# Kernel optimization log

Measured on AMD Instinct MI355X. Metric: run time of the kernel, lower is better.

The kernel has to match this reference:

```python
import math
import jax, jax.numpy as jnp
import numpy as np

NUM_HEADS = 16
ROTARY_BASE = 10000.0
FMIN = -3.4028234663852886e+38  # torch uses -FLT_MAX as the blocked logit value


def setup_inputs() -> dict:
    key = jax.random.key(0)
    ks = jax.random.split(key, 4)
    B, S, D = 2, 2048, 2048
    x = jax.random.normal(ks[0], (B, S, D), dtype=jnp.float32)
    mask = jnp.ones((B, S), dtype=bool)
    # Linear params stored as [in, out] (transpose of torch's [out, in])
    w_in = jax.random.normal(ks[1], (D, 3 * D), dtype=jnp.float32) * 0.02
    b_in = jnp.zeros((3 * D,), dtype=jnp.float32)
    w_out = jax.random.normal(ks[2], (D, D), dtype=jnp.float32) * 0.02
    b_out = jnp.zeros((D,), dtype=jnp.float32)
    return {"x": x, "mask": mask, "w_in": w_in, "b_in": b_in,
            "w_out": w_out, "b_out": b_out}


def _rotate_half(t):
    # curated-transformers RotaryEmbeddings._rotate: [-x2, x1]
    h = t.shape[-1] // 2
    return jnp.concatenate([-t[..., h:], t[..., :h]], axis=-1)


def _rope_cos_sin(seq_len, width):
    # theta_i = base^(-2i/d); m_theta duplicated (rotate-half / NeoX layout)
    theta = ROTARY_BASE ** (-jnp.arange(0, width, 2, dtype=jnp.float32) / width)
    m_theta = jnp.arange(seq_len, dtype=jnp.float32)[:, None] * theta[None, :]
    m_theta = jnp.concatenate([m_theta, m_theta], axis=-1)  # [S, width]
    return jnp.cos(m_theta), jnp.sin(m_theta)


def reference(x, mask, w_in, b_in, w_out, b_out):
    B, S, D = x.shape
    H = NUM_HEADS
    Dh = D // H

    proj = x @ w_in + b_in                       # [B, S, 3D]
    q, k, v = jnp.split(proj, 3, axis=-1)
    split = lambda t: t.reshape(B, S, H, Dh).transpose(0, 2, 1, 3)  # [B,H,S,Dh]
    q, k, v = split(q), split(k), split(v)

    # rotary_fraction == 1.0 -> full-head rotary, default positions 0..S-1
    cos, sin = _rope_cos_sin(S, Dh)              # [S, Dh]
    cos = cos[None, None]
    sin = sin[None, None]
    q = cos * q + sin * _rotate_half(q)
    k = cos * k + sin * _rotate_half(k)

    scores = jnp.einsum('bhqd,bhkd->bhqk', q, k) / math.sqrt(Dh)
    # causal mask (use_causal_mask=True): strictly upper triangle blocked
    causal = jnp.triu(jnp.full((S, S), FMIN, dtype=scores.dtype), k=1)
    scores = scores + causal[None, None]
    # padding mask: (1 - mask) * -FLT_MAX, broadcast over heads and queries
    logit_mask = (1.0 - mask.astype(scores.dtype)) * FMIN
    scores = scores + logit_mask[:, None, None, :]

    attn_w = jax.nn.softmax(scores, axis=-1)
    attn = jnp.einsum('bhqk,bhkd->bhqd', attn_w, v)  # dropout_prob=0 (eval)
    attn = attn.transpose(0, 2, 1, 3).reshape(B, S, D)  # combine_heads
    return attn @ w_out + b_out
```

## Files before the change

kernel.cpp:

```cpp
#include <hip/hip_runtime.h>

typedef unsigned short ushort_t;
typedef unsigned int u32;
typedef short bf16x8 __attribute__((ext_vector_type(8)));
typedef float f32x4 __attribute__((ext_vector_type(4)));

__device__ __forceinline__ ushort_t f2bf(float f) {
  u32 u = __float_as_uint(f);
  u += 0x7FFFu + ((u >> 16) & 1u);
  return (ushort_t)(u >> 16);
}
__device__ __forceinline__ float bf2f(ushort_t h) {
  return __uint_as_float(((u32)h) << 16);
}

__device__ __forceinline__ void async_cp16(const void* g, void* l) {
  __builtin_amdgcn_global_load_lds(
      (const u32 __attribute__((address_space(1)))*)(unsigned long long)g,
      (u32 __attribute__((address_space(3)))*)(u32)(unsigned long long)l,
      16, 0, 0);
}

#define MFMA_BF16(a, b, c) __builtin_amdgcn_mfma_f32_16x16x32_bf16((a), (b), (c), 0, 0, 0)

#define KFENCE() __asm__ __volatile__("" ::: "memory")
#define KBAR()                    \
  do {                            \
    KFENCE();                     \
    __builtin_amdgcn_s_barrier(); \
    KFENCE();                     \
  } while (0)

__global__ void cvt_bf16_k(const float* __restrict__ in, ushort_t* __restrict__ out, int n4) {
  int i = blockIdx.x * blockDim.x + threadIdx.x;
  if (i >= n4) return;
  float4 v = ((const float4*)in)[i];
  unsigned long long p = (unsigned long long)f2bf(v.x)
                       | ((unsigned long long)f2bf(v.y) << 16)
                       | ((unsigned long long)f2bf(v.z) << 32)
                       | ((unsigned long long)f2bf(v.w) << 48);
  ((unsigned long long*)out)[i] = p;
}

__global__ void transpose_cvt_k(const float* __restrict__ in, ushort_t* __restrict__ out,
                                int R, int C) {
  __shared__ float t[32][33];
  int c0 = blockIdx.x * 32, r0 = blockIdx.y * 32;
  int tx = threadIdx.x, ty = threadIdx.y;
#pragma unroll
  for (int i = 0; i < 4; ++i)
    t[ty + i * 8][tx] = in[(size_t)(r0 + ty + i * 8) * C + c0 + tx];
  __syncthreads();
#pragma unroll
  for (int i = 0; i < 4; ++i)
    out[(size_t)(c0 + ty + i * 8) * R + r0 + tx] = f2bf(t[tx][ty + i * 8]);
}

__global__ void rope_swz_k(const ushort_t* __restrict__ q, const ushort_t* __restrict__ k,
                           ushort_t* __restrict__ qs, ushort_t* __restrict__ ks) {
  int row = blockIdx.x * 2 + (threadIdx.x >> 7);
  int d = threadIdx.x & 127;
  int s = row & 2047;
  int i = d & 63;
  float theta = __expf(-(float)i * 0.14391156831212876f);
  float mt = (float)s * theta;
  float sn, cs;
  sincosf(mt, &sn, &cs);
  size_t base = (size_t)row * 128;
  float qd = bf2f(q[base + d]), qp = bf2f(q[base + (d ^ 64)]);
  float kd = bf2f(k[base + d]), kp = bf2f(k[base + (d ^ 64)]);
  float rq = (d < 64) ? -qp : qp;
  float rk = (d < 64) ? -kp : kp;
  size_t bhb = (size_t)(row >> 11) * 262144;
  size_t qoff = bhb + (size_t)((s >> 5) * 4096 + ((d >> 5) * 2 + ((s >> 4) & 1)) * 512 +
                               (((d >> 3) & 3) * 16 + (s & 15)) * 8 + (d & 7));
  size_t koff = bhb + (size_t)((s >> 6) * 8192 + (d >> 5) * 2048 + ((s >> 4) & 3) * 512 +
                               ((d >> 3) & 3) * 128 + (s & 15) * 8 + (d & 7));
  qs[qoff] = f2bf(cs * qd + sn * rq);
  ks[koff] = f2bf(cs * kd + sn * rk);
}

template <int MODE>
__global__ __launch_bounds__(256, 2) void gemm_bt_k(
    const ushort_t* __restrict__ A, const ushort_t* __restrict__ Bt,
    const float* __restrict__ bias, float* __restrict__ Cout,
    ushort_t* __restrict__ Qd, ushort_t* __restrict__ Kd, ushort_t* __restrict__ Vd,
    int M, int N, int K) {
  __shared__ ushort_t As[128 * 32];
  __shared__ ushort_t Bs[128 * 32];

  const int tid = threadIdx.x;
  const int w = tid >> 6, lane = tid & 63;
  const int quad = lane >> 4, l15 = lane & 15;
  const int m0 = blockIdx.y * 128, n0 = blockIdx.x * 128;
  const int wr = w >> 1, wc = w & 1;

  f32x4 acc[4][4] = {};

  for (int k0 = 0; k0 < K; k0 += 32) {
#pragma unroll
    for (int i = 0; i < 2; ++i) {
      int slot = (w * 2 + i) * 64 + lane;
      int row = slot >> 2, seg = slot & 3;
      async_cp16(A + (size_t)(m0 + row) * K + k0 + seg * 8, As + (size_t)(w * 2 + i) * 512);
      async_cp16(Bt + (size_t)(n0 + row) * K + k0 + seg * 8, Bs + (size_t)(w * 2 + i) * 512);
    }
    __syncthreads();

    bf16x8 a[4], b[4];
#pragma unroll
    for (int mt = 0; mt < 4; ++mt)
      a[mt] = *(const bf16x8*)(As + (wr * 64 + mt * 16 + l15) * 32 + quad * 8);
#pragma unroll
    for (int nt = 0; nt < 4; ++nt)
      b[nt] = *(const bf16x8*)(Bs + (wc * 64 + nt * 16 + l15) * 32 + quad * 8);
#pragma unroll
    for (int mt = 0; mt < 4; ++mt)
#pragma unroll
      for (int nt = 0; nt < 4; ++nt)
        acc[mt][nt] = MFMA_BF16(a[mt], b[nt], acc[mt][nt]);
    __syncthreads();
  }

  if (MODE == 0) {
#pragma unroll
    for (int mt = 0; mt < 4; ++mt)
#pragma unroll
      for (int nt = 0; nt < 4; ++nt) {
        int col = n0 + wc * 64 + nt * 16 + l15;
        float bv = bias[col];
#pragma unroll
        for (int r = 0; r < 4; ++r) {
          int row = m0 + wr * 64 + mt * 16 + quad * 4 + r;
          Cout[(size_t)row * N + col] = acc[mt][nt][r] + bv;
        }
      }
  } else {
#pragma unroll
    for (int mt = 0; mt < 4; ++mt)
#pragma unroll
      for (int nt = 0; nt < 4; ++nt) {
        int col = n0 + wc * 64 + nt * 16 + l15;
        int which = col >> 11;
        int rem = col & 2047;
        int h = rem >> 7, d = rem & 127;
        float bv = bias[col];
#pragma unroll
        for (int r = 0; r < 4; ++r) {
          int row = m0 + wr * 64 + mt * 16 + quad * 4 + r;
          int bb = row >> 11, s = row & 2047;
          size_t bhb = (size_t)(bb * 16 + h) * 262144;
          ushort_t val = f2bf(acc[mt][nt][r] + bv);
          if (which == 2) {
            size_t off = bhb + (size_t)((s >> 6) * 8192 + ((s >> 5) & 1) * 4096 +
                                        (d >> 4) * 512 + ((s >> 3) & 3) * 128 +
                                        (d & 15) * 8 + (s & 7));
            Vd[off] = val;
          } else {
            ushort_t* dst = (which == 0) ? Qd : Kd;
            dst[bhb + (size_t)s * 128 + d] = val;
          }
        }
      }
  }
}

__device__ __forceinline__ void stage_tile64(const ushort_t* gs, ushort_t* lbase,
                                             int w, int K, int k0) {
  ushort_t* l = lbase + w * 512;
#pragma unroll
  for (int c = 0; c < 4; ++c)
    async_cp16(gs + (size_t)(c * 64) * K + k0, l + c * 4096);
}

template <int MODE>
__global__ __launch_bounds__(512, 2) void gemm256_k(
    const ushort_t* __restrict__ A, const ushort_t* __restrict__ Bt,
    const float* __restrict__ bias, float* __restrict__ Cout,
    ushort_t* __restrict__ Qd, ushort_t* __restrict__ Kd, ushort_t* __restrict__ Vd,
    int M, int N, int K) {
  __shared__ ushort_t As[2][16384];
  __shared__ ushort_t Bs[2][16384];

  const int tid = threadIdx.x;
  const int w = tid >> 6, lane = tid & 63;
  const int quad = lane >> 4, l15 = lane & 15;
  const int wr = w >> 2, wc = w & 3;
  const int m0 = blockIdx.y * 256, n0 = blockIdx.x * 256;

  const int rr = (w << 3) + (lane >> 3);
  const int sw = ((lane & 7) ^ ((lane >> 3) & 7)) << 3;
  const ushort_t* Ags = A + (size_t)(m0 + rr) * K + sw;
  const ushort_t* Bgs = Bt + (size_t)(n0 + rr) * K + sw;

  f32x4 acc[8][4] = {};

  stage_tile64(Ags, As[0], w, K, 0);
  stage_tile64(Bgs, Bs[0], w, K, 0);
  stage_tile64(Ags, As[1], w, K, 64);
  stage_tile64(Bgs, Bs[1], w, K, 64);
  __asm__ __volatile__("s_waitcnt vmcnt(8)" ::: "memory");
  KBAR();

  const int NT = K >> 6;

  for (int t = 0; t < NT; ++t) {
    const ushort_t* Ab = As[t & 1];
    const ushort_t* Bb = Bs[t & 1];
    const bool pre = (t + 2) < NT;
    const int kpre = (t + 2) << 6;

    bf16x8 a[4][2], b0[2][2], b1[2][2];

#pragma unroll
    for (int q = 0; q < 4; ++q)
#pragma unroll
      for (int kk = 0; kk < 2; ++kk) {
        int row = wr * 128 + q * 16 + l15;
        int gr = ((kk << 2) | quad) ^ (l15 & 7);
        a[q][kk] = *(const bf16x8*)(Ab + row * 64 + gr * 8);
      }
#pragma unroll
    for (int n2 = 0; n2 < 2; ++n2)
#pragma unroll
      for (int kk = 0; kk < 2; ++kk) {
        int row = wc * 64 + n2 * 16 + l15;
        int gr = ((kk << 2) | quad) ^ (l15 & 7);
        b0[n2][kk] = *(const bf16x8*)(Bb + row * 64 + gr * 8);
      }
    KBAR();
    __builtin_amdgcn_s_setprio(1);
#pragma unroll
    for (int q = 0; q < 4; ++q)
#pragma unroll
      for (int n2 = 0; n2 < 2; ++n2)
#pragma unroll
        for (int kk = 0; kk < 2; ++kk)
          acc[q][n2] = MFMA_BF16(a[q][kk], b0[n2][kk], acc[q][n2]);
    __builtin_amdgcn_s_setprio(0);
    KBAR();

#pragma unroll
    for (int n2 = 0; n2 < 2; ++n2)
#pragma unroll
      for (int kk = 0; kk < 2; ++kk) {
        int row = wc * 64 + 32 + n2 * 16 + l15;
        int gr = ((kk << 2) | quad) ^ (l15 & 7);
        b1[n2][kk] = *(const bf16x8*)(Bb + row * 64 + gr * 8);
      }
    KBAR();
    __builtin_amdgcn_s_setprio(1);
#pragma unroll
    for (int q = 0; q < 4; ++q)
#pragma unroll
      for (int n2 = 0; n2 < 2; ++n2)
#pragma unroll
        for (int kk = 0; kk < 2; ++kk)
          acc[q][2 + n2] = MFMA_BF16(a[q][kk], b1[n2][kk], acc[q][2 + n2]);
    __builtin_amdgcn_s_setprio(0);
    KBAR();

#pragma unroll
    for (int q = 0; q < 4; ++q)
#pragma unroll
      for (int kk = 0; kk < 2; ++kk) {
        int row = wr * 128 + 64 + q * 16 + l15;
        int gr = ((kk << 2) | quad) ^ (l15 & 7);
        a[q][kk] = *(const bf16x8*)(Ab + row * 64 + gr * 8);
      }
    if (pre) stage_tile64(Bgs, Bs[t & 1], w, K, kpre);
    KBAR();
    __builtin_amdgcn_s_setprio(1);
#pragma unroll
    for (int q = 0; q < 4; ++q)
#pragma unroll
      for (int n2 = 0; n2 < 2; ++n2)
#pragma unroll
        for (int kk = 0; kk < 2; ++kk)
          acc[4 + q][n2] = MFMA_BF16(a[q][kk], b0[n2][kk], acc[4 + q][n2]);
    __builtin_amdgcn_s_setprio(0);
    KBAR();

    if (pre) stage_tile64(Ags, As[t & 1], w, K, kpre);
    KBAR();
    __builtin_amdgcn_s_setprio(1);
#pragma unroll
    for (int q = 0; q < 4; ++q)
#pragma unroll
      for (int n2 = 0; n2 < 2; ++n2)
#pragma unroll
        for (int kk = 0; kk < 2; ++kk)
          acc[4 + q][2 + n2] = MFMA_BF16(a[q][kk], b1[n2][kk], acc[4 + q][2 + n2]);
    __builtin_amdgcn_s_setprio(0);
    if (pre) {
      __asm__ __volatile__("s_waitcnt vmcnt(8)" ::: "memory");
    } else {
      __asm__ __volatile__("s_waitcnt vmcnt(0)" ::: "memory");
    }
    KBAR();
  }

  if (MODE == 0) {
#pragma unroll
    for (int mt = 0; mt < 8; ++mt)
#pragma unroll
      for (int nt = 0; nt < 4; ++nt) {
        int col = n0 + wc * 64 + nt * 16 + l15;
        float bv = bias[col];
#pragma unroll
        for (int r = 0; r < 4; ++r) {
          int row = m0 + wr * 128 + mt * 16 + quad * 4 + r;
          Cout[(size_t)row * N + col] = acc[mt][nt][r] + bv;
        }
      }
  } else {
#pragma unroll
    for (int mt = 0; mt < 8; ++mt)
#pragma unroll
      for (int nt = 0; nt < 4; ++nt) {
        int col = n0 + wc * 64 + nt * 16 + l15;
        int which = col >> 11;
        int rem = col & 2047;
        int h = rem >> 7, d = rem & 127;
        float bv = bias[col];
#pragma unroll
        for (int r = 0; r < 4; ++r) {
          int row = m0 + wr * 128 + mt * 16 + quad * 4 + r;
          int bb = row >> 11, s = row & 2047;
          size_t bhb = (size_t)(bb * 16 + h) * 262144;
          ushort_t val = f2bf(acc[mt][nt][r] + bv);
          if (which == 2) {
            size_t off = bhb + (size_t)((s >> 6) * 8192 + ((s >> 5) & 1) * 4096 +
                                        (d >> 4) * 512 + ((s >> 3) & 3) * 128 +
                                        (d & 15) * 8 + (s & 7));
            Vd[off] = val;
          } else {
            ushort_t* dst = (which == 0) ? Qd : Kd;
            dst[bhb + (size_t)s * 128 + d] = val;
          }
        }
      }
  }
}

__global__ __launch_bounds__(256, 2) void attn_flash_k(
    const ushort_t* __restrict__ Qs, const ushort_t* __restrict__ Ks,
    const ushort_t* __restrict__ Vs, ushort_t* __restrict__ Ob) {
  __shared__ ushort_t Ps[4][2048];

  const int tid = threadIdx.x, w = tid >> 6, lane = tid & 63;
  const int quad = lane >> 4, l15 = lane & 15;
  const int bh = blockIdx.y;
  const int b = bh >> 4, h = bh & 15;
  const int xe = ((bh >> 4) & 1) ? (15 - (int)blockIdx.x) : (int)blockIdx.x;
  const int idx = xe * 4 + w;
  const int g = (idx & 1) ? (idx >> 1) : (63 - (idx >> 1));
  const int q0 = g * 32;
  const int ktmax = g >> 1;
  const size_t bhb = (size_t)bh * 262144;
  const float scale2 = 0.08838834764831845f * 1.44269504088896340f;

  bf16x8 qa[2][4];
#pragma unroll
  for (int mt = 0; mt < 2; ++mt)
#pragma unroll
    for (int kq = 0; kq < 4; ++kq)
      qa[mt][kq] = *(const bf16x8*)(Qs + bhb + g * 4096 + (kq * 2 + mt) * 512 + lane * 8);

  f32x4 o[2][8] = {};
  float mi[2][4], li[2][4];
#pragma unroll
  for (int mt = 0; mt < 2; ++mt)
#pragma unroll
    for (int r = 0; r < 4; ++r) { mi[mt][r] = -1e30f; li[mt][r] = 0.f; }

  ushort_t* Pw = Ps[w];

  for (int kt = 0; kt <= ktmax; ++kt) {
    const int k0 = kt * 64;
    const ushort_t* kbase = Ks + bhb + kt * 8192;
    const ushort_t* vbase = Vs + bhb + kt * 8192;

    bf16x8 kb[4][4];
#pragma unroll
    for (int kq = 0; kq < 4; ++kq)
#pragma unroll
      for (int nt = 0; nt < 4; ++nt)
        kb[kq][nt] = *(const bf16x8*)(kbase + (kq * 4 + nt) * 512 + lane * 8);

    f32x4 sa[2][4] = {};
#pragma unroll
    for (int kq = 0; kq < 4; ++kq)
#pragma unroll
      for (int nt = 0; nt < 4; ++nt) {
        sa[0][nt] = MFMA_BF16(qa[0][kq], kb[kq][nt], sa[0][nt]);
        sa[1][nt] = MFMA_BF16(qa[1][kq], kb[kq][nt], sa[1][nt]);
      }

    bf16x8 vb[2][8];
#pragma unroll
    for (int ks = 0; ks < 2; ++ks)
#pragma unroll
      for (int nt = 0; nt < 8; ++nt)
        vb[ks][nt] = *(const bf16x8*)(vbase + (ks * 8 + nt) * 512 + lane * 8);

    const bool diag = (kt == ktmax);
#pragma unroll
    for (int mt = 0; mt < 2; ++mt) {
#pragma unroll
      for (int r = 0; r < 4; ++r) {
        int qg = q0 + mt * 16 + quad * 4 + r;
        float sv[4];
        float rmax = -1e30f;
#pragma unroll
        for (int nt = 0; nt < 4; ++nt) {
          float vv = sa[mt][nt][r] * scale2;
          if (diag) { int kgc = k0 + nt * 16 + l15; if (kgc > qg) vv = -1e30f; }
          sv[nt] = vv;
          rmax = fmaxf(rmax, vv);
        }
        rmax = fmaxf(rmax, __shfl_xor(rmax, 1));
        rmax = fmaxf(rmax, __shfl_xor(rmax, 2));
        rmax = fmaxf(rmax, __shfl_xor(rmax, 4));
        rmax = fmaxf(rmax, __shfl_xor(rmax, 8));
        float mnew = fmaxf(mi[mt][r], rmax);
        float alpha = exp2f(mi[mt][r] - mnew);
        float psum = 0.f;
#pragma unroll
        for (int nt = 0; nt < 4; ++nt) {
          float p = exp2f(sv[nt] - mnew);
          psum += p;
          Pw[(mt * 2 + (nt >> 1)) * 512 + (nt & 1) * 256 + (l15 >> 3) * 128 +
             quad * 32 + r * 8 + (l15 & 7)] = f2bf(p);
        }
        psum += __shfl_xor(psum, 1);
        psum += __shfl_xor(psum, 2);
        psum += __shfl_xor(psum, 4);
        psum += __shfl_xor(psum, 8);
        li[mt][r] = li[mt][r] * alpha + psum;
        mi[mt][r] = mnew;
#pragma unroll
        for (int nt = 0; nt < 8; ++nt) o[mt][nt][r] *= alpha;
      }
    }

    __asm__ __volatile__("" ::: "memory");

#pragma unroll
    for (int ks = 0; ks < 2; ++ks) {
      bf16x8 pa0 = *(const bf16x8*)(Pw + (0 * 2 + ks) * 512 + lane * 8);
      bf16x8 pa1 = *(const bf16x8*)(Pw + (1 * 2 + ks) * 512 + lane * 8);
#pragma unroll
      for (int nt = 0; nt < 8; ++nt) {
        o[0][nt] = MFMA_BF16(pa0, vb[ks][nt], o[0][nt]);
        o[1][nt] = MFMA_BF16(pa1, vb[ks][nt], o[1][nt]);
      }
    }
  }

#pragma unroll
  for (int mt = 0; mt < 2; ++mt)
#pragma unroll
    for (int r = 0; r < 4; ++r) {
      float inv = 1.f / li[mt][r];
      int s = q0 + mt * 16 + quad * 4 + r;
      size_t rowbase = ((size_t)b * 2048 + s) * 2048 + h * 128;
#pragma unroll
      for (int nt = 0; nt < 8; ++nt)
        Ob[rowbase + nt * 16 + l15] = f2bf(o[mt][nt][r] * inv);
    }
}

extern "C" void kernel_launch(void* const* d_in, const int* in_sizes, int n_in,
                              void* d_out, int out_size, void* d_ws, size_t ws_size,
                              hipStream_t stream) {
  const float* x     = (const float*)d_in[0];
  const float* w_in  = (const float*)d_in[2];
  const float* b_in  = (const float*)d_in[3];
  const float* w_out = (const float*)d_in[4];
  const float* b_out = (const float*)d_in[5];
  float* out = (float*)d_out;

  ushort_t* x_bf    = (ushort_t*)d_ws;
  ushort_t* w_in_t  = x_bf + 8388608;
  ushort_t* w_out_t = w_in_t + 12582912;
  ushort_t* q       = w_out_t + 4194304;
  ushort_t* k       = q + 8388608;
  ushort_t* vswz    = k + 8388608;

  ushort_t* qswz = x_bf;
  ushort_t* kswz = w_in_t;
  ushort_t* attn = q;

  cvt_bf16_k<<<dim3(8192), dim3(256), 0, stream>>>(x, x_bf, 2097152);
  transpose_cvt_k<<<dim3(192, 64), dim3(32, 8), 0, stream>>>(w_in, w_in_t, 2048, 6144);
  transpose_cvt_k<<<dim3(64, 64), dim3(32, 8), 0, stream>>>(w_out, w_out_t, 2048, 2048);
  gemm256_k<1><<<dim3(24, 16), dim3(512), 0, stream>>>(
      x_bf, w_in_t, b_in, nullptr, q, k, vswz, 4096, 6144, 2048);
  rope_swz_k<<<dim3(32768), dim3(256), 0, stream>>>(q, k, qswz, kswz);
  attn_flash_k<<<dim3(16, 32), dim3(256), 0, stream>>>(qswz, kswz, vswz, attn);
  gemm_bt_k<0><<<dim3(16, 32), dim3(256), 0, stream>>>(
      attn, w_out_t, b_out, out, nullptr, nullptr, nullptr, 4096, 2048, 2048);
}
```

Measured before the change: 471.7 us.

## Use one-wave attention blocks with K-tile register prefetch and new block ordering

The attention kernel now launches single-wavefront blocks (2048 blocks of 64 threads) instead of four waves per block, and linearizes the grid so consecutive blocks cycle across batch-heads, with long and short query tiles interleaved for load balance. The key loop is unrolled by two with ping-pong registers, so half of the next K tile is loaded during the current tile's softmax. This aims to hide global load latency and cut tail imbalance, at the cost of more registers and many more small blocks per CU.

```diff
diff --git a/kernel.cpp b/kernel.cpp
--- a/kernel.cpp
+++ b/kernel.cpp
@@ -343,18 +343,18 @@
   }
 }
 
-__global__ __launch_bounds__(256, 2) void attn_flash_k(
+__global__ __launch_bounds__(64, 2) void attn_flash_k(
     const ushort_t* __restrict__ Qs, const ushort_t* __restrict__ Ks,
     const ushort_t* __restrict__ Vs, ushort_t* __restrict__ Ob) {
-  __shared__ ushort_t Ps[4][2048];
-
-  const int tid = threadIdx.x, w = tid >> 6, lane = tid & 63;
+  __shared__ ushort_t Pw[2048];
+
+  const int lane = threadIdx.x & 63;
   const int quad = lane >> 4, l15 = lane & 15;
-  const int bh = blockIdx.y;
+  const int n = blockIdx.x;
+  const int bh = (n & 7) * 4 + ((n >> 3) & 3);
+  const int sx = n >> 5;
+  const int g = (sx & 1) ? (sx >> 1) : (63 - (sx >> 1));
   const int b = bh >> 4, h = bh & 15;
-  const int xe = ((bh >> 4) & 1) ? (15 - (int)blockIdx.x) : (int)blockIdx.x;
-  const int idx = xe * 4 + w;
-  const int g = (idx & 1) ? (idx >> 1) : (63 - (idx >> 1));
   const int q0 = g * 32;
   const int ktmax = g >> 1;
   const size_t bhb = (size_t)bh * 262144;
@@ -374,89 +374,108 @@
 #pragma unroll
     for (int r = 0; r < 4; ++r) { mi[mt][r] = -1e30f; li[mt][r] = 0.f; }
 
-  ushort_t* Pw = Ps[w];
-
-  for (int kt = 0; kt <= ktmax; ++kt) {
-    const int k0 = kt * 64;
-    const ushort_t* kbase = Ks + bhb + kt * 8192;
-    const ushort_t* vbase = Vs + bhb + kt * 8192;
-
-    bf16x8 kb[4][4];
-#pragma unroll
-    for (int kq = 0; kq < 4; ++kq)
+  bf16x8 kpA[2][4], kpB[2][4];
+  {
+    const ushort_t* kbase = Ks + bhb;
+#pragma unroll
+    for (int kq = 0; kq < 2; ++kq)
 #pragma unroll
       for (int nt = 0; nt < 4; ++nt)
-        kb[kq][nt] = *(const bf16x8*)(kbase + (kq * 4 + nt) * 512 + lane * 8);
-
-    f32x4 sa[2][4] = {};
-#pragma unroll
-    for (int kq = 0; kq < 4; ++kq)
-#pragma unroll
-      for (int nt = 0; nt < 4; ++nt) {
-        sa[0][nt] = MFMA_BF16(qa[0][kq], kb[kq][nt], sa[0][nt]);
-        sa[1][nt] = MFMA_BF16(qa[1][kq], kb[kq][nt], sa[1][nt]);
-      }
-
-    bf16x8 vb[2][8];
-#pragma unroll
-    for (int ks = 0; ks < 2; ++ks)
-#pragma unroll
-      for (int nt = 0; nt < 8; ++nt)
-        vb[ks][nt] = *(const bf16x8*)(vbase + (ks * 8 + nt) * 512 + lane * 8);
-
-    const bool diag = (kt == ktmax);
-#pragma unroll
-    for (int mt = 0; mt < 2; ++mt) {
-#pragma unroll
-      for (int r = 0; r < 4; ++r) {
-        int qg = q0 + mt * 16 + quad * 4 + r;
-        float sv[4];
-        float rmax = -1e30f;
-#pragma unroll
-        for (int nt = 0; nt < 4; ++nt) {
-          float vv = sa[mt][nt][r] * scale2;
-          if (diag) { int kgc = k0 + nt * 16 + l15; if (kgc > qg) vv = -1e30f; }
-          sv[nt] = vv;
-          rmax = fmaxf(rmax, vv);
-        }
-        rmax = fmaxf(rmax, __shfl_xor(rmax, 1));
-        rmax = fmaxf(rmax, __shfl_xor(rmax, 2));
-        rmax = fmaxf(rmax, __shfl_xor(rmax, 4));
-        rmax = fmaxf(rmax, __shfl_xor(rmax, 8));
-        float mnew = fmaxf(mi[mt][r], rmax);
-        float alpha = exp2f(mi[mt][r] - mnew);
-        float psum = 0.f;
-#pragma unroll
-        for (int nt = 0; nt < 4; ++nt) {
-          float p = exp2f(sv[nt] - mnew);
-          psum += p;
-          Pw[(mt * 2 + (nt >> 1)) * 512 + (nt & 1) * 256 + (l15 >> 3) * 128 +
-             quad * 32 + r * 8 + (l15 & 7)] = f2bf(p);
-        }
-        psum += __shfl_xor(psum, 1);
-        psum += __shfl_xor(psum, 2);
-        psum += __shfl_xor(psum, 4);
-        psum += __shfl_xor(psum, 8);
-        li[mt][r] = li[mt][r] * alpha + psum;
-        mi[mt][r] = mnew;
-#pragma unroll
-        for (int nt = 0; nt < 8; ++nt) o[mt][nt][r] *= alpha;
-      }
-    }
-
-    __asm__ __volatile__("" ::: "memory");
-
-#pragma unroll
-    for (int ks = 0; ks < 2; ++ks) {
-      bf16x8 pa0 = *(const bf16x8*)(Pw + (0 * 2 + ks) * 512 + lane * 8);
-      bf16x8 pa1 = *(const bf16x8*)(Pw + (1 * 2 + ks) * 512 + lane * 8);
-#pragma unroll
-      for (int nt = 0; nt < 8; ++nt) {
-        o[0][nt] = MFMA_BF16(pa0, vb[ks][nt], o[0][nt]);
-        o[1][nt] = MFMA_BF16(pa1, vb[ks][nt], o[1][nt]);
-      }
-    }
-  }
+        kpA[kq][nt] = *(const bf16x8*)(kbase + (kq * 4 + nt) * 512 + lane * 8);
+  }
+
+  int kt = 0;
+
+#define ATTN_TILE_BODY(KP_CUR, KP_NXT)                                          \
+  {                                                                             \
+    const int k0 = kt * 64;                                                     \
+    const ushort_t* kbase = Ks + bhb + (size_t)kt * 8192;                       \
+    const ushort_t* vbase = Vs + bhb + (size_t)kt * 8192;                       \
+             \
+    bf16x8 kb23[2][4];                                                          \
+    _Pragma("unroll") for (int kq = 0; kq < 2; ++kq)                            \
+      _Pragma("unroll") for (int nt = 0; nt < 4; ++nt)                          \
+        kb23[kq][nt] =                                                          \
+            *(const bf16x8*)(kbase + ((kq + 2) * 4 + nt) * 512 + lane * 8);     \
+    f32x4 sa[2][4] = {};                                                        \
+    _Pragma("unroll") for (int kq = 0; kq < 2; ++kq)                            \
+      _Pragma("unroll") for (int nt = 0; nt < 4; ++nt) {                        \
+        sa[0][nt] = MFMA_BF16(qa[0][kq], KP_CUR[kq][nt], sa[0][nt]);            \
+        sa[1][nt] = MFMA_BF16(qa[1][kq], KP_CUR[kq][nt], sa[1][nt]);            \
+      }                                                                         \
+    _Pragma("unroll") for (int kq = 0; kq < 2; ++kq)                            \
+      _Pragma("unroll") for (int nt = 0; nt < 4; ++nt) {                        \
+        sa[0][nt] = MFMA_BF16(qa[0][kq + 2], kb23[kq][nt], sa[0][nt]);          \
+        sa[1][nt] = MFMA_BF16(qa[1][kq + 2], kb23[kq][nt], sa[1][nt]);          \
+      }                                                                         \
+              \
+    bf16x8 vb[2][8];                                                            \
+    _Pragma("unroll") for (int ks = 0; ks < 2; ++ks)                            \
+      _Pragma("unroll") for (int nt = 0; nt < 8; ++nt)                          \
+        vb[ks][nt] = *(const bf16x8*)(vbase + (ks * 8 + nt) * 512 + lane * 8);  \
+    const bool diag = (kt == ktmax);                                            \
+    _Pragma("unroll") for (int mt = 0; mt < 2; ++mt) {                          \
+      _Pragma("unroll") for (int r = 0; r < 4; ++r) {                           \
+        int qg = q0 + mt * 16 + quad * 4 + r;                                   \
+        float sv[4];                                                            \
+        float rmax = -1e30f;                                                    \
+        _Pragma("unroll") for (int nt = 0; nt < 4; ++nt) {                      \
+          float vv = sa[mt][nt][r] * scale2;                                    \
+          if (diag) {                                                           \
+            int kgc = k0 + nt * 16 + l15;                                       \
+            if (kgc > qg) vv = -1e30f;                                          \
+          }                                                                     \
+          sv[nt] = vv;                                                          \
+          rmax = fmaxf(rmax, vv);                                               \
+        }                                                                       \
+        rmax = fmaxf(rmax, __shfl_xor(rmax, 1));                                \
+        rmax = fmaxf(rmax, __shfl_xor(rmax, 2));                                \
+        rmax = fmaxf(rmax, __shfl_xor(rmax, 4));                                \
+        rmax = fmaxf(rmax, __shfl_xor(rmax, 8));                                \
+        float mnew = fmaxf(mi[mt][r], rmax);                                    \
+        float alpha = exp2f(mi[mt][r] - mnew);                                  \
+        float psum = 0.f;                                                       \
+        _Pragma("unroll") for (int nt = 0; nt < 4; ++nt) {                      \
+          float p = exp2f(sv[nt] - mnew);                                       \
+          psum += p;                                                            \
+          Pw[(mt * 2 + (nt >> 1)) * 512 + (nt & 1) * 256 + (l15 >> 3) * 128 +   \
+             quad * 32 + r * 8 + (l15 & 7)] = f2bf(p);                          \
+        }                                                                       \
+        psum += __shfl_xor(psum, 1);                                            \
+        psum += __shfl_xor(psum, 2);                                            \
+        psum += __shfl_xor(psum, 4);                                            \
+        psum += __shfl_xor(psum, 8);                                            \
+        li[mt][r] = li[mt][r] * alpha + psum;                                   \
+        mi[mt][r] = mnew;                                                       \
+        _Pragma("unroll") for (int nt = 0; nt < 8; ++nt) o[mt][nt][r] *= alpha; \
+      }                                                                         \
+    }                                                                           \
+            \
+    if (kt < ktmax) {                                                           \
+      _Pragma("unroll") for (int kq = 0; kq < 2; ++kq)                          \
+        _Pragma("unroll") for (int nt = 0; nt < 4; ++nt)                        \
+          KP_NXT[kq][nt] =                                                      \
+              *(const bf16x8*)(kbase + 8192 + (kq * 4 + nt) * 512 + lane * 8);  \
+    }                                                                           \
+           \
+    __asm__ __volatile__("" ::: "memory");                                      \
+    _Pragma("unroll") for (int ks = 0; ks < 2; ++ks) {                          \
+      bf16x8 pa0 = *(const bf16x8*)(Pw + (0 * 2 + ks) * 512 + lane * 8);        \
+      bf16x8 pa1 = *(const bf16x8*)(Pw + (1 * 2 + ks) * 512 + lane * 8);        \
+      _Pragma("unroll") for (int nt = 0; nt < 8; ++nt) {                        \
+        o[0][nt] = MFMA_BF16(pa0, vb[ks][nt], o[0][nt]);                        \
+        o[1][nt] = MFMA_BF16(pa1, vb[ks][nt], o[1][nt]);                        \
+      }                                                                         \
+    }                                                                           \
+  }
+
+  while (true) {
+    ATTN_TILE_BODY(kpA, kpB);
+    if (++kt > ktmax) break;
+    ATTN_TILE_BODY(kpB, kpA);
+    if (++kt > ktmax) break;
+  }
+#undef ATTN_TILE_BODY
 
 #pragma unroll
   for (int mt = 0; mt < 2; ++mt)
@@ -498,7 +517,7 @@
   gemm256_k<1><<<dim3(24, 16), dim3(512), 0, stream>>>(
       x_bf, w_in_t, b_in, nullptr, q, k, vswz, 4096, 6144, 2048);
   rope_swz_k<<<dim3(32768), dim3(256), 0, stream>>>(q, k, qswz, kswz);
-  attn_flash_k<<<dim3(16, 32), dim3(256), 0, stream>>>(qswz, kswz, vswz, attn);
+  attn_flash_k<<<dim3(2048), dim3(64), 0, stream>>>(qswz, kswz, vswz, attn);
   gemm_bt_k<0><<<dim3(16, 32), dim3(256), 0, stream>>>(
       attn, w_out_t, b_out, out, nullptr, nullptr, nullptr, 4096, 2048, 2048);
 }
```

New measurement: 633.8 us. 34.4% more time.
